# Performance work log

Hardware: AMD Instinct MI355X
Metric: run time of the kernel (lower is better)

Reference implementation:

```python
import jax, jax.numpy as jnp
import numpy as np

N_NODES = 100000
N_EDGES = 2000000
IN_X, IN_E, HID, OUT = 32, 64, 128, 64


def setup_inputs() -> dict:
    key = jax.random.key(0)
    ks = jax.random.split(key, 12)
    def w(k, shape, fan_in):
        return jax.random.normal(k, shape, dtype=jnp.float32) / np.sqrt(fan_in)
    x = jax.random.normal(ks[0], (N_NODES, IN_X), dtype=jnp.float32)
    edge_index = jax.random.randint(ks[1], (2, N_EDGES), 0, N_NODES)
    return {
        "x": x,
        "edge_index": edge_index,
        # initial_lin: in_x -> in_e
        "W0": w(ks[2], (IN_X, IN_E), IN_X),
        "b0": jnp.zeros((IN_E,), jnp.float32),
        # SAGEConv1: lin_l (aggregated neighbors, with bias), lin_r (self, no bias)
        "W1l": w(ks[3], (IN_E, HID), IN_E),
        "b1l": jnp.zeros((HID,), jnp.float32),
        "W1r": w(ks[4], (IN_E, HID), IN_E),
        # SAGEConv2
        "W2l": w(ks[5], (HID, OUT), HID),
        "b2l": jnp.zeros((OUT,), jnp.float32),
        "W2r": w(ks[6], (HID, OUT), HID),
        # pred head: 2*out -> 1
        "Wp": w(ks[7], (2 * OUT, 1), 2 * OUT),
        "bp": jnp.zeros((1,), jnp.float32),
    }


def _sage_conv(x, edge_index, Wl, bl, Wr):
    # PyG SAGEConv, aggr='mean': out = lin_l(mean_{j in N(i)} x_j) + lin_r(x_i)
    src, dst = edge_index[0], edge_index[1]
    n = x.shape[0]
    msg = x[src]                                   # [E, F] gather
    ssum = jax.ops.segment_sum(msg, dst, num_segments=n)          # [N, F]
    cnt = jax.ops.segment_sum(jnp.ones((edge_index.shape[1],), x.dtype), dst,
                              num_segments=n)                      # [N]
    aggr = ssum / jnp.maximum(cnt, 1.0)[:, None]
    return aggr @ Wl + bl + x @ Wr


def reference(x, edge_index, W0, b0, W1l, b1l, W1r, W2l, b2l, W2r, Wp, bp):
    h = x @ W0 + b0                                # initial_lin
    h = jax.nn.relu(_sage_conv(h, edge_index, W1l, b1l, W1r))
    # dropout p=0.5 is identity in eval mode
    h = _sage_conv(h, edge_index, W2l, b2l, W2r)   # [N, OUT]
    src, dst = edge_index[0], edge_index[1]
    combined = jnp.concatenate([h[src], h[dst]], axis=1)  # [E, 2*OUT]
    raw = (combined @ Wp + bp)[:, 0]               # squeeze -> [E]
    return raw, jax.nn.sigmoid(raw)
```

## Files before the change

kernel.cpp:

```cpp
#include <hip/hip_runtime.h>
#include <hip/hip_bf16.h>
#include <hip/hip_fp16.h>


#define IN_X 32
#define IN_E 64
#define HID 128
#define OUTF 64

#define BSHIFT 7
#define BSZ 128
#define NBP 1024
#define CHUNK 4096
#define CAP 4096

typedef _Float16 f16x8 __attribute__((ext_vector_type(8)));
typedef float f32x4 __attribute__((ext_vector_type(4)));

__device__ __forceinline__ float2 h2f2(uint v) {
  __half2 h = *reinterpret_cast<__half2*>(&v);
  return __half22float2(h);
}
__device__ __forceinline__ __half2 u2h(uint v) {
  return *reinterpret_cast<__half2*>(&v);
}

__global__ __launch_bounds__(256) void k_prep(
    const float* __restrict__ W0, const float* __restrict__ b0,
    const float* __restrict__ W1l, const float* __restrict__ b1l,
    const float* __restrict__ W1r,
    const float* __restrict__ W2l, const float* __restrict__ W2r,
    const float* __restrict__ b2l, const float* __restrict__ Wp,
    __half* __restrict__ U1T, __half* __restrict__ U2T, float* __restrict__ c1,
    float* __restrict__ svecs, float* __restrict__ hb,
    const float* __restrict__ x, __half* __restrict__ xh, int xtotal) {
  const int blk = blockIdx.x;
  if (blk < 32) {
    __shared__ float sW0[IN_X * IN_E];
    for (int t = threadIdx.x; t < IN_X * IN_E; t += 256) sW0[t] = W0[t];
    __syncthreads();
    const int o = blk * 256 + threadIdx.x;
    const int hf = o >> 12;
    const int rem = o & 4095;
    const int j = rem >> 5, i = rem & 31;
    const float* W = hf ? W1r : W1l;
    float u = 0.f;
    #pragma unroll 8
    for (int k = 0; k < IN_E; ++k) u += sW0[i * IN_E + k] * W[k * HID + j];
    (hf ? U2T : U1T)[j * IN_X + i] = __float2half(u);
  } else if (blk == 32) {
    const int j = threadIdx.x;
    if (j < HID) {
      float cv = b1l[j];
      for (int k = 0; k < IN_E; ++k)
        cv += b0[k] * (W1l[k * HID + j] + W1r[k * HID + j]);
      c1[j] = cv;
    } else if (j == HID || j == HID + 1) {
      const float* w = Wp + (j - HID) * OUTF;
      float s = 0.f;
      for (int k = 0; k < OUTF; ++k) s += b2l[k] * w[k];
      hb[j - HID] = s;
    }
  } else if (blk == 33 || blk == 34) {
    __shared__ float sW[HID * OUTF];
    const float* W = (blk == 33) ? W2l : W2r;
    for (int t = threadIdx.x; t < HID * OUTF; t += 256) sW[t] = W[t];
    __syncthreads();
    const int vec = threadIdx.x >> 7;
    const int j = threadIdx.x & 127;
    const float* w = Wp + vec * OUTF;
    float s = 0.f;
    #pragma unroll 8
    for (int k = 0; k < OUTF; ++k) s += sW[j * OUTF + k] * w[k];
    svecs[(blk - 33) * 256 + vec * 128 + j] = s;
  } else {
    int i = ((blk - 35) * 256 + threadIdx.x) * 8;
    if (i < xtotal) {
      float4 a = *(const float4*)(x + i);
      float4 b = *(const float4*)(x + i + 4);
      __half2 h0 = __floats2half2_rn(a.x, a.y);
      __half2 h1 = __floats2half2_rn(a.z, a.w);
      __half2 h2 = __floats2half2_rn(b.x, b.y);
      __half2 h3 = __floats2half2_rn(b.z, b.w);
      uint4 o = { *(uint*)&h0, *(uint*)&h1, *(uint*)&h2, *(uint*)&h3 };
      *(uint4*)(xh + i) = o;
    }
  }
}

__global__ __launch_bounds__(512) void k_scatfuse(const int* __restrict__ src,
    const int* __restrict__ dst, int* __restrict__ gcursor,
    uint* __restrict__ bucketData, int E) {
  __shared__ int hist[NBP];
  const int cblk = blockIdx.x;
  for (int i = threadIdx.x; i < NBP; i += 512) hist[i] = 0;
  __syncthreads();
  const int base = cblk * CHUNK;
  int d[CHUNK / 512], s[CHUNK / 512];
  #pragma unroll
  for (int k = 0; k < CHUNK / 512; ++k) {
    int e = base + k * 512 + threadIdx.x;
    d[k] = (e < E) ? dst[e] : -1;
    s[k] = (e < E) ? src[e] : 0;
  }
  #pragma unroll
  for (int k = 0; k < CHUNK / 512; ++k)
    if (d[k] >= 0) atomicAdd(&hist[d[k] >> BSHIFT], 1);
  __syncthreads();
  for (int i = threadIdx.x; i < NBP; i += 512) {
    int h = hist[i];
    hist[i] = (h > 0) ? atomicAdd(&gcursor[i], h) : 0;
  }
  __syncthreads();
  #pragma unroll
  for (int k = 0; k < CHUNK / 512; ++k) {
    if (d[k] >= 0) {
      int bkt = d[k] >> BSHIFT;
      int pos = atomicAdd(&hist[bkt], 1);
      if (pos < CAP)
        bucketData[(size_t)bkt * CAP + pos] =
            ((uint)s[k] << BSHIFT) | (uint)(d[k] & (BSZ - 1));
    }
  }
}

__global__ __launch_bounds__(512) void k_baggr32s(const __half* __restrict__ feat,
    const uint* __restrict__ bucketData, const int* __restrict__ gcnt,
    __half* __restrict__ aggr, uint* __restrict__ gorder,
    int* __restrict__ gns, int* __restrict__ gne, int N) {
  constexpr int FW = IN_X;
  constexpr int LPR = FW / 4;
  constexpr int RPW = 64 / LPR;
  __shared__ int nodeStart[BSZ + 1];
  __shared__ int cursor[BSZ];
  __shared__ int order[CAP];
  const int b = blockIdx.x;
  const int tid = threadIdx.x;
  const int lane = tid & 63, wid = tid >> 6;
  const int e0 = b * CAP;
  const int cnt = min(gcnt[b], CAP);

  if (tid < BSZ) cursor[tid] = 0;
  __syncthreads();
  for (int i = tid; i < cnt; i += 512)
    atomicAdd(&cursor[bucketData[e0 + i] & (BSZ - 1)], 1);
  __syncthreads();

  if (wid == 0) {
    int v0 = cursor[lane], v1 = cursor[64 + lane];
    int x0 = v0, x1 = v1;
    #pragma unroll
    for (int s = 1; s < 64; s <<= 1) {
      int y0 = __shfl_up(x0, s, 64);
      int y1 = __shfl_up(x1, s, 64);
      if (lane >= s) { x0 += y0; x1 += y1; }
    }
    int tot0 = __shfl(x0, 63, 64);
    nodeStart[lane] = x0 - v0;
    nodeStart[64 + lane] = tot0 + x1 - v1;
    if (lane == 63) nodeStart[BSZ] = tot0 + x1;
  }
  __syncthreads();
  if (tid < BSZ) cursor[tid] = nodeStart[tid];
  __syncthreads();

  for (int i = tid; i < cnt; i += 512) {
    uint p = bucketData[e0 + i];
    int pos = atomicAdd(&cursor[p & (BSZ - 1)], 1);
    order[pos] = (int)(p >> BSHIFT);
  }
  __syncthreads();

  for (int i = tid; i < cnt; i += 512) gorder[e0 + i] = (uint)order[i];
  if (tid < BSZ) {
    const int n = b * BSZ + tid;
    if (n < N) { gns[n] = e0 + nodeStart[tid]; gne[n] = e0 + nodeStart[tid + 1]; }
  }

  const int nodes = min(BSZ, N - b * BSZ);
  const int g = lane / LPR, e = lane % LPR;
  for (int n = wid; n < nodes; n += 8) {
    const int s = nodeStart[n], t = nodeStart[n + 1];
    __half2 ax = __floats2half2_rn(0.f, 0.f), ay = ax;
    int j = s;
    for (; j + 2 * RPW <= t; j += 2 * RPW) {
      int r0 = order[j + g], r1 = order[j + RPW + g];
      uint2 v0 = ((const uint2*)(feat + (size_t)r0 * FW))[e];
      uint2 v1 = ((const uint2*)(feat + (size_t)r1 * FW))[e];
      ax = __hadd2(ax, __hadd2(u2h(v0.x), u2h(v1.x)));
      ay = __hadd2(ay, __hadd2(u2h(v0.y), u2h(v1.y)));
    }
    for (; j < t; j += RPW) {
      if (j + g < t) {
        int r = order[j + g];
        uint2 v = ((const uint2*)(feat + (size_t)r * FW))[e];
        ax = __hadd2(ax, u2h(v.x));
        ay = __hadd2(ay, u2h(v.y));
      }
    }
    float2 fx = __half22float2(ax), fy = __half22float2(ay);
    float4 acc = {fx.x, fx.y, fy.x, fy.y};
    #pragma unroll
    for (int m = LPR; m < 64; m <<= 1) {
      acc.x += __shfl_xor(acc.x, m, 64);
      acc.y += __shfl_xor(acc.y, m, 64);
      acc.z += __shfl_xor(acc.z, m, 64);
      acc.w += __shfl_xor(acc.w, m, 64);
    }
    if (g == 0) {
      float inv = 1.f / fmaxf((float)(t - s), 1.f);
      __half2 o0 = __floats2half2_rn(acc.x * inv, acc.y * inv);
      __half2 o1 = __floats2half2_rn(acc.z * inv, acc.w * inv);
      uint2 o = { *(uint*)&o0, *(uint*)&o1 };
      ((uint2*)(aggr + ((size_t)(b * BSZ + n)) * FW))[e] = o;
    }
  }
}

__global__ __launch_bounds__(256) void k_conv1fused(
    const __half* __restrict__ axm, const __half* __restrict__ xh,
    const __half* __restrict__ U1T, const __half* __restrict__ U2T,
    const float* __restrict__ c1, const float* __restrict__ svecs,
    float2* __restrict__ tsd, float2* __restrict__ ssd, int N) {
  __shared__ _Float16 tile[4][16 * HID];
  __shared__ float svec[512];
  const int lane = threadIdx.x & 63;
  const int wid = threadIdx.x >> 6;
  const int row0 = blockIdx.x * 64 + wid * 16;
  const int lr = lane & 15;
  const int lk = (lane >> 4) * 8;

  for (int i = threadIdx.x; i < 512; i += 256) svec[i] = svecs[i];

  {
    f16x8 b1[8], b2[8];
    #pragma unroll
    for (int ct = 0; ct < 8; ++ct) {
      const int c = ct * 16 + lr;
      b1[ct] = *(const f16x8*)((const _Float16*)U1T + (size_t)c * IN_X + lk);
      b2[ct] = *(const f16x8*)((const _Float16*)U2T + (size_t)c * IN_X + lk);
    }
    f32x4 acc[8];
    #pragma unroll
    for (int ct = 0; ct < 8; ++ct) {
      float bv = c1[ct * 16 + lr];
      acc[ct] = (f32x4){bv, bv, bv, bv};
    }
    const int rA = min(row0 + lr, N - 1);
    f16x8 a1 = *(const f16x8*)((const _Float16*)axm + (size_t)rA * IN_X + lk);
    f16x8 a2 = *(const f16x8*)((const _Float16*)xh + (size_t)rA * IN_X + lk);
    #pragma unroll
    for (int ct = 0; ct < 8; ++ct)
      acc[ct] = __builtin_amdgcn_mfma_f32_16x16x32_f16(a1, b1[ct], acc[ct], 0, 0, 0);
    #pragma unroll
    for (int ct = 0; ct < 8; ++ct)
      acc[ct] = __builtin_amdgcn_mfma_f32_16x16x32_f16(a2, b2[ct], acc[ct], 0, 0, 0);
    #pragma unroll
    for (int ct = 0; ct < 8; ++ct) {
      #pragma unroll
      for (int r = 0; r < 4; ++r) {
        const int row = (lane >> 4) * 4 + r;
        const int col = ct * 16 + lr;
        int idx = (row * HID + col) ^ ((row & 7) << 3);
        tile[wid][idx] = (_Float16)fmaxf(acc[ct][r], 0.f);
      }
    }
  }
  __syncthreads();

  const int row = lane & 15, q = lane >> 4;
  float ts = 0.f, td = 0.f, ss = 0.f, sd = 0.f;
  #pragma unroll
  for (int t = 0; t < 4; ++t) {
    const int col = q * 32 + t * 8;
    int idx = (row * HID + col) ^ ((row & 7) << 3);
    f16x8 h = *(const f16x8*)&tile[wid][idx];
    #pragma unroll
    for (int i = 0; i < 8; ++i) {
      float hv = (float)h[i];
      ts += hv * svec[col + i];
      td += hv * svec[128 + col + i];
      ss += hv * svec[256 + col + i];
      sd += hv * svec[384 + col + i];
    }
  }
  ts += __shfl_xor(ts, 16, 64); ts += __shfl_xor(ts, 32, 64);
  td += __shfl_xor(td, 16, 64); td += __shfl_xor(td, 32, 64);
  ss += __shfl_xor(ss, 16, 64); ss += __shfl_xor(ss, 32, 64);
  sd += __shfl_xor(sd, 16, 64); sd += __shfl_xor(sd, 32, 64);
  if (q == 0) {
    const int grow = row0 + row;
    if (grow < N) {
      tsd[grow] = make_float2(ts, td);
      ssd[grow] = make_float2(ss, sd);
    }
  }
}

__global__ __launch_bounds__(256) void k_scalagg(const float2* __restrict__ tsd,
    const float2* __restrict__ ssd, const int* __restrict__ gns,
    const int* __restrict__ gne, const uint* __restrict__ gorder,
    const float* __restrict__ hb,
    float* __restrict__ gs, float* __restrict__ gd, int N) {
  const int n = blockIdx.x * 256 + threadIdx.x;
  if (n >= N) return;
  const int s = gns[n], t = gne[n];
  float ax = 0.f, ay = 0.f;
  int j = s;
  for (; j + 4 <= t; j += 4) {
    int r0 = (int)gorder[j],     r1 = (int)gorder[j + 1];
    int r2 = (int)gorder[j + 2], r3 = (int)gorder[j + 3];
    float2 a = tsd[r0], b = tsd[r1], c = tsd[r2], d = tsd[r3];
    ax += (a.x + b.x) + (c.x + d.x);
    ay += (a.y + b.y) + (c.y + d.y);
  }
  for (; j < t; ++j) {
    float2 a = tsd[(int)gorder[j]];
    ax += a.x; ay += a.y;
  }
  const float inv = 1.f / fmaxf((float)(t - s), 1.f);
  const float2 sv = ssd[n];
  gs[n] = sv.x + ax * inv + hb[0];
  gd[n] = sv.y + ay * inv + hb[1];
}

__global__ __launch_bounds__(256) void k_edge(const float* __restrict__ gs,
    const float* __restrict__ gd, const int* __restrict__ srcI,
    const int* __restrict__ dstI, const float* __restrict__ bp,
    float* __restrict__ out, int E) {
  int e = blockIdx.x * 256 + threadIdx.x;
  if (e >= E) return;
  float raw = gs[srcI[e]] + gd[dstI[e]] + bp[0];
  out[e] = raw;
  out[(size_t)E + e] = 1.f / (1.f + expf(-raw));
}

extern "C" void kernel_launch(void* const* d_in, const int* in_sizes, int n_in,
                              void* d_out, int out_size, void* d_ws, size_t ws_size,
                              hipStream_t stream) {
  const float* x   = (const float*)d_in[0];
  const int*   ei  = (const int*)d_in[1];
  const float* W0  = (const float*)d_in[2];
  const float* b0  = (const float*)d_in[3];
  const float* W1l = (const float*)d_in[4];
  const float* b1l = (const float*)d_in[5];
  const float* W1r = (const float*)d_in[6];
  const float* W2l = (const float*)d_in[7];
  const float* b2l = (const float*)d_in[8];
  const float* W2r = (const float*)d_in[9];
  const float* Wp  = (const float*)d_in[10];
  const float* bp  = (const float*)d_in[11];

  const int N = in_sizes[0] / IN_X;
  const int E = in_sizes[1] / 2;
  const int* srcI = ei;
  const int* dstI = ei + E;
  float* out = (float*)d_out;

  const int NB = (N + BSZ - 1) >> BSHIFT;
  const int nchunk = (E + CHUNK - 1) / CHUNK;

  __half* xh  = (__half*)d_ws;
  __half* axm = xh + (size_t)N * IN_X;
  float2* tsd = (float2*)(axm + (size_t)N * IN_X);
  float2* ssd = tsd + N;
  float* gs   = (float*)(ssd + N);
  float* gd   = gs + N;
  uintptr_t wp = ((uintptr_t)(gd + N) + 15) & ~(uintptr_t)15;
  __half* U1T  = (__half*)wp;
  __half* U2T  = U1T + HID * IN_X;
  float* c1    = (float*)(U2T + HID * IN_X);
  float* svecs = c1 + HID;
  float* hb    = svecs + 512;
  int* gcursor = (int*)(hb + 2);
  int* gns     = gcursor + NBP;
  int* gne     = gns + N + 1;
  uint* bucketData = (uint*)(gne + N);
  uint* gorder     = bucketData + (size_t)NBP * CAP;

  hipMemsetAsync(gcursor, 0, sizeof(int) * NBP, stream);

  const int xblocks = (N * IN_X / 8 + 255) / 256;
  k_prep<<<35 + xblocks, 256, 0, stream>>>(W0, b0, W1l, b1l, W1r, W2l, W2r,
                                           b2l, Wp, U1T, U2T, c1, svecs, hb,
                                           x, xh, N * IN_X);
  k_scatfuse<<<nchunk, 512, 0, stream>>>(srcI, dstI, gcursor, bucketData, E);
  k_baggr32s<<<NB, 512, 0, stream>>>(xh, bucketData, gcursor, axm, gorder, gns, gne, N);
  k_conv1fused<<<(N + 63) / 64, 256, 0, stream>>>(axm, xh, U1T, U2T, c1,
                                                  svecs, tsd, ssd, N);
  k_scalagg<<<(N + 255) / 256, 256, 0, stream>>>(tsd, ssd, gns, gne, gorder,
                                                 hb, gs, gd, N);
  k_edge<<<(E + 255) / 256, 256, 0, stream>>>(gs, gd, srcI, dstI, bp, out, E);
}
```

Measured before the change: 129.6 us.

## Split neighbor aggregation into two source-range passes and fold memset into prep

Within each destination bucket, edges are now sorted by destination and by whether the source node lies in the lower or upper half of the node range. The aggregation runs two passes, first over low-half sources and then over high-half sources, so the gathered feature working set in each phase is smaller and more likely to stay in cache. The partial sums are kept in LDS between the passes, and the cross-lane reduction now runs in half precision rather than float. The gcursor memset is also moved into an extra k_prep block so one API call disappears, at the cost of an extra barrier phase and a little precision in the reduction.

```diff
diff --git a/kernel.cpp b/kernel.cpp
--- a/kernel.cpp
+++ b/kernel.cpp
@@ -23,6 +23,9 @@
 }
 __device__ __forceinline__ __half2 u2h(uint v) {
   return *reinterpret_cast<__half2*>(&v);
+}
+__device__ __forceinline__ uint h2u(__half2 h) {
+  return *reinterpret_cast<uint*>(&h);
 }
 
 __global__ __launch_bounds__(256) void k_prep(
@@ -32,7 +35,7 @@
     const float* __restrict__ W2l, const float* __restrict__ W2r,
     const float* __restrict__ b2l, const float* __restrict__ Wp,
     __half* __restrict__ U1T, __half* __restrict__ U2T, float* __restrict__ c1,
-    float* __restrict__ svecs, float* __restrict__ hb,
+    float* __restrict__ svecs, float* __restrict__ hb, int* __restrict__ gcursor,
     const float* __restrict__ x, __half* __restrict__ xh, int xtotal) {
   const int blk = blockIdx.x;
   if (blk < 32) {
@@ -73,8 +76,11 @@
     #pragma unroll 8
     for (int k = 0; k < OUTF; ++k) s += sW[j * OUTF + k] * w[k];
     svecs[(blk - 33) * 256 + vec * 128 + j] = s;
+  } else if (blk == 35) {
+    #pragma unroll
+    for (int k = 0; k < NBP / 256; ++k) gcursor[k * 256 + threadIdx.x] = 0;
   } else {
-    int i = ((blk - 35) * 256 + threadIdx.x) * 8;
+    int i = ((blk - 36) * 256 + threadIdx.x) * 8;
     if (i < xtotal) {
       float4 a = *(const float4*)(x + i);
       float4 b = *(const float4*)(x + i + 4);
@@ -127,46 +133,51 @@
 __global__ __launch_bounds__(512) void k_baggr32s(const __half* __restrict__ feat,
     const uint* __restrict__ bucketData, const int* __restrict__ gcnt,
     __half* __restrict__ aggr, uint* __restrict__ gorder,
-    int* __restrict__ gns, int* __restrict__ gne, int N) {
+    int* __restrict__ gns, int* __restrict__ gne, int N, int Nhalf) {
   constexpr int FW = IN_X;
-  constexpr int LPR = FW / 4;
-  constexpr int RPW = 64 / LPR;
-  __shared__ int nodeStart[BSZ + 1];
-  __shared__ int cursor[BSZ];
+  __shared__ int nodeStart[2 * BSZ + 1];
+  __shared__ int cursor[2 * BSZ];
   __shared__ int order[CAP];
+  __shared__ uint2 stash[BSZ * 8];
   const int b = blockIdx.x;
   const int tid = threadIdx.x;
   const int lane = tid & 63, wid = tid >> 6;
   const int e0 = b * CAP;
   const int cnt = min(gcnt[b], CAP);
 
-  if (tid < BSZ) cursor[tid] = 0;
-  __syncthreads();
-  for (int i = tid; i < cnt; i += 512)
-    atomicAdd(&cursor[bucketData[e0 + i] & (BSZ - 1)], 1);
-  __syncthreads();
-
-  if (wid == 0) {
-    int v0 = cursor[lane], v1 = cursor[64 + lane];
-    int x0 = v0, x1 = v1;
-    #pragma unroll
-    for (int s = 1; s < 64; s <<= 1) {
-      int y0 = __shfl_up(x0, s, 64);
-      int y1 = __shfl_up(x1, s, 64);
-      if (lane >= s) { x0 += y0; x1 += y1; }
-    }
-    int tot0 = __shfl(x0, 63, 64);
-    nodeStart[lane] = x0 - v0;
-    nodeStart[64 + lane] = tot0 + x1 - v1;
-    if (lane == 63) nodeStart[BSZ] = tot0 + x1;
-  }
-  __syncthreads();
-  if (tid < BSZ) cursor[tid] = nodeStart[tid];
-  __syncthreads();
-
+  for (int i = tid; i < 2 * BSZ; i += 512) cursor[i] = 0;
+  __syncthreads();
   for (int i = tid; i < cnt; i += 512) {
     uint p = bucketData[e0 + i];
-    int pos = atomicAdd(&cursor[p & (BSZ - 1)], 1);
+    int key = ((p & (BSZ - 1)) << 1) | ((int)(p >> BSHIFT) >= Nhalf ? 1 : 0);
+    atomicAdd(&cursor[key], 1);
+  }
+  __syncthreads();
+
+  if (wid == 0) {
+    int carry = 0;
+    #pragma unroll
+    for (int seg = 0; seg < 4; ++seg) {
+      int v = cursor[seg * 64 + lane];
+      int x = v;
+      #pragma unroll
+      for (int s = 1; s < 64; s <<= 1) {
+        int y = __shfl_up(x, s, 64);
+        if (lane >= s) x += y;
+      }
+      nodeStart[seg * 64 + lane] = carry + x - v;
+      carry += __shfl(x, 63, 64);
+    }
+    if (lane == 0) nodeStart[2 * BSZ] = carry;
+  }
+  __syncthreads();
+  for (int i = tid; i < 2 * BSZ; i += 512) cursor[i] = nodeStart[i];
+  __syncthreads();
+
+  for (int i = tid; i < cnt; i += 512) {
+    uint p = bucketData[e0 + i];
+    int key = ((p & (BSZ - 1)) << 1) | ((int)(p >> BSHIFT) >= Nhalf ? 1 : 0);
+    int pos = atomicAdd(&cursor[key], 1);
     order[pos] = (int)(p >> BSHIFT);
   }
   __syncthreads();
@@ -174,23 +185,27 @@
   for (int i = tid; i < cnt; i += 512) gorder[e0 + i] = (uint)order[i];
   if (tid < BSZ) {
     const int n = b * BSZ + tid;
-    if (n < N) { gns[n] = e0 + nodeStart[tid]; gne[n] = e0 + nodeStart[tid + 1]; }
+    if (n < N) {
+      gns[n] = e0 + nodeStart[2 * tid];
+      gne[n] = e0 + nodeStart[2 * tid + 2];
+    }
   }
 
   const int nodes = min(BSZ, N - b * BSZ);
-  const int g = lane / LPR, e = lane % LPR;
+  const int g = lane >> 3, e = lane & 7;
+
   for (int n = wid; n < nodes; n += 8) {
-    const int s = nodeStart[n], t = nodeStart[n + 1];
+    const int s = nodeStart[2 * n], t = nodeStart[2 * n + 1];
     __half2 ax = __floats2half2_rn(0.f, 0.f), ay = ax;
     int j = s;
-    for (; j + 2 * RPW <= t; j += 2 * RPW) {
-      int r0 = order[j + g], r1 = order[j + RPW + g];
+    for (; j + 16 <= t; j += 16) {
+      int r0 = order[j + g], r1 = order[j + 8 + g];
       uint2 v0 = ((const uint2*)(feat + (size_t)r0 * FW))[e];
       uint2 v1 = ((const uint2*)(feat + (size_t)r1 * FW))[e];
       ax = __hadd2(ax, __hadd2(u2h(v0.x), u2h(v1.x)));
       ay = __hadd2(ay, __hadd2(u2h(v0.y), u2h(v1.y)));
     }
-    for (; j < t; j += RPW) {
+    for (; j < t; j += 8) {
       if (j + g < t) {
         int r = order[j + g];
         uint2 v = ((const uint2*)(feat + (size_t)r * FW))[e];
@@ -198,20 +213,49 @@
         ay = __hadd2(ay, u2h(v.y));
       }
     }
-    float2 fx = __half22float2(ax), fy = __half22float2(ay);
-    float4 acc = {fx.x, fx.y, fy.x, fy.y};
-    #pragma unroll
-    for (int m = LPR; m < 64; m <<= 1) {
-      acc.x += __shfl_xor(acc.x, m, 64);
-      acc.y += __shfl_xor(acc.y, m, 64);
-      acc.z += __shfl_xor(acc.z, m, 64);
-      acc.w += __shfl_xor(acc.w, m, 64);
+    #pragma unroll
+    for (int m = 8; m < 64; m <<= 1) {
+      ax = __hadd2(ax, u2h((uint)__shfl_xor((int)h2u(ax), m, 64)));
+      ay = __hadd2(ay, u2h((uint)__shfl_xor((int)h2u(ay), m, 64)));
+    }
+    if (g == 0) stash[n * 8 + e] = make_uint2(h2u(ax), h2u(ay));
+  }
+  __syncthreads();
+
+  for (int n = wid; n < nodes; n += 8) {
+    const int s = nodeStart[2 * n + 1], t = nodeStart[2 * n + 2];
+    __half2 ax = __floats2half2_rn(0.f, 0.f), ay = ax;
+    int j = s;
+    for (; j + 16 <= t; j += 16) {
+      int r0 = order[j + g], r1 = order[j + 8 + g];
+      uint2 v0 = ((const uint2*)(feat + (size_t)r0 * FW))[e];
+      uint2 v1 = ((const uint2*)(feat + (size_t)r1 * FW))[e];
+      ax = __hadd2(ax, __hadd2(u2h(v0.x), u2h(v1.x)));
+      ay = __hadd2(ay, __hadd2(u2h(v0.y), u2h(v1.y)));
+    }
+    for (; j < t; j += 8) {
+      if (j + g < t) {
+        int r = order[j + g];
+        uint2 v = ((const uint2*)(feat + (size_t)r * FW))[e];
+        ax = __hadd2(ax, u2h(v.x));
+        ay = __hadd2(ay, u2h(v.y));
+      }
+    }
+    #pragma unroll
+    for (int m = 8; m < 64; m <<= 1) {
+      ax = __hadd2(ax, u2h((uint)__shfl_xor((int)h2u(ax), m, 64)));
+      ay = __hadd2(ay, u2h((uint)__shfl_xor((int)h2u(ay), m, 64)));
     }
     if (g == 0) {
-      float inv = 1.f / fmaxf((float)(t - s), 1.f);
-      __half2 o0 = __floats2half2_rn(acc.x * inv, acc.y * inv);
-      __half2 o1 = __floats2half2_rn(acc.z * inv, acc.w * inv);
-      uint2 o = { *(uint*)&o0, *(uint*)&o1 };
+      uint2 st = stash[n * 8 + e];
+      ax = __hadd2(ax, u2h(st.x));
+      ay = __hadd2(ay, u2h(st.y));
+      const int deg = nodeStart[2 * n + 2] - nodeStart[2 * n];
+      float inv = 1.f / fmaxf((float)deg, 1.f);
+      float2 fx = __half22float2(ax), fy = __half22float2(ay);
+      __half2 o0 = __floats2half2_rn(fx.x * inv, fx.y * inv);
+      __half2 o1 = __floats2half2_rn(fy.x * inv, fy.y * inv);
+      uint2 o = { h2u(o0), h2u(o1) };
       ((uint2*)(aggr + ((size_t)(b * BSZ + n)) * FW))[e] = o;
     }
   }
@@ -378,14 +422,13 @@
   uint* bucketData = (uint*)(gne + N);
   uint* gorder     = bucketData + (size_t)NBP * CAP;
 
-  hipMemsetAsync(gcursor, 0, sizeof(int) * NBP, stream);
-
   const int xblocks = (N * IN_X / 8 + 255) / 256;
-  k_prep<<<35 + xblocks, 256, 0, stream>>>(W0, b0, W1l, b1l, W1r, W2l, W2r,
+  k_prep<<<36 + xblocks, 256, 0, stream>>>(W0, b0, W1l, b1l, W1r, W2l, W2r,
                                            b2l, Wp, U1T, U2T, c1, svecs, hb,
-                                           x, xh, N * IN_X);
+                                           gcursor, x, xh, N * IN_X);
   k_scatfuse<<<nchunk, 512, 0, stream>>>(srcI, dstI, gcursor, bucketData, E);
-  k_baggr32s<<<NB, 512, 0, stream>>>(xh, bucketData, gcursor, axm, gorder, gns, gne, N);
+  k_baggr32s<<<NB, 512, 0, stream>>>(xh, bucketData, gcursor, axm, gorder,
+                                     gns, gne, N, N / 2);
   k_conv1fused<<<(N + 63) / 64, 256, 0, stream>>>(axm, xh, U1T, U2T, c1,
                                                   svecs, tsd, ssd, N);
   k_scalagg<<<(N + 255) / 256, 256, 0, stream>>>(tsd, ssd, gns, gne, gorder,
```

Result: no change. 128.9 us (-0.5%).
